# Kernel optimization log

Measured on AMD Instinct MI355X. Metric: run time of the kernel, lower is better.

Reference implementation:

```python
import jax, jax.numpy as jnp
import numpy as np

D = 256        # model_dim
E = 4          # num_experts
H = 8          # attention heads
L = 8          # layers
P = 4          # patch size
IMG = 128
B = 8
NUM_CLASSES = 10
T = (IMG // P) ** 2  # 1024 tokens


def _ln(x, g, b):
    mu = jnp.mean(x, -1, keepdims=True)
    var = jnp.mean((x - mu) ** 2, -1, keepdims=True)
    return (x - mu) * jax.lax.rsqrt(var + 1e-5) * g + b


def setup_inputs() -> dict:
    key = jax.random.key(0)
    ks = jax.random.split(key, 24)
    n = lambda k, s, sc=0.02: jax.random.normal(k, s, jnp.float32) * sc
    return {
        "x": jax.random.normal(ks[0], (B, 3, IMG, IMG), jnp.float32),
        "patch_w": n(ks[1], (D, 3, P, P), 0.1),
        "patch_b": n(ks[2], (D,), 0.01),
        "pos_emb": n(ks[3], (1, T, D), 0.02),
        "router_w": n(ks[4], (E, D), 0.05),
        "router_b": n(ks[5], (E,), 0.01),
        "ln1_g": jnp.ones((L, D), jnp.float32),
        "ln1_b": jnp.zeros((L, D), jnp.float32),
        "q_w": n(ks[6], (L, D, D), 0.05),
        "q_b": n(ks[7], (L, D), 0.01),
        "k_w": n(ks[8], (L, D, D), 0.05),
        "k_b": n(ks[9], (L, D), 0.01),
        "v_w": n(ks[10], (L, D, D), 0.05),
        "v_b": n(ks[11], (L, D), 0.01),
        "o_w": n(ks[12], (L, D, D), 0.05),
        "o_b": n(ks[13], (L, D), 0.01),
        "ln2_g": jnp.ones((L, D), jnp.float32),
        "ln2_b": jnp.zeros((L, D), jnp.float32),
        "l1_w": n(ks[14], (L, 4 * D, D), 0.05),
        "l1_b": n(ks[15], (L, 4 * D), 0.01),
        "l2_w": n(ks[16], (L, D, 4 * D), 0.05),
        "l2_b": n(ks[17], (L, D), 0.01),
        "head_w": n(ks[18], (NUM_CLASSES, D), 0.05),
        "head_b": n(ks[19], (NUM_CLASSES,), 0.01),
        "alpha": jnp.full((1,), 0.5, jnp.float32),
    }


def reference(x, patch_w, patch_b, pos_emb, router_w, router_b, ln1_g, ln1_b,
              q_w, q_b, k_w, k_b, v_w, v_b, o_w, o_b, ln2_g, ln2_b,
              l1_w, l1_b, l2_w, l2_b, head_w, head_b, alpha):
    b = x.shape[0]
    # patch embed: Conv2d(3, D, P, stride=P)
    h = jax.lax.conv_general_dilated(x, patch_w, (P, P), 'VALID',
                                     dimension_numbers=('NCHW', 'OIHW', 'NCHW'))
    h = h + patch_b[None, :, None, None]
    tok = h.reshape(b, D, -1).transpose(0, 2, 1) + pos_emb   # [B,T,D]
    t = tok.shape[1]
    n_per = t // E  # uniform capacity: floor(T * 1/E)
    raw_prob = jax.nn.softmax(tok @ router_w.T + router_b, axis=-1)  # [B,T,E]
    # greedy routing: expert e takes top n_per of remaining tokens, rows zeroed after
    prob = raw_prob
    bidx = jnp.arange(b)[:, None]
    blocks, pblocks = [], []
    for e in range(E):
        _, idx = jax.lax.top_k(prob[:, :, e], n_per)            # [B,n_per]
        blocks.append(jnp.take_along_axis(tok, idx[:, :, None], axis=1))
        pblocks.append(jnp.take_along_axis(raw_prob, idx[:, :, None], axis=1))
        sel = jnp.zeros((b, t), prob.dtype).at[bidx, idx].set(1.0)
        prob = prob * (1.0 - sel)[:, :, None]
    xs = jnp.concatenate(blocks, axis=1)    # [B,T,D] expert-sorted
    rp = jnp.concatenate(pblocks, axis=1)   # [B,T,E]

    widths = [D // 2 ** e for e in range(E)]  # [256,128,64,32]
    scale = D ** -0.5                         # note: model_dim, not head_dim
    dh = D // H
    for l in range(L):
        # ---- nested-expert MHSA ----
        xn = _ln(xs, ln1_g[l], ln1_b[l])
        qs, ks_, vs = [], [], []
        for e in range(E):
            m = widths[e]
            blk = xn[:, e * n_per:(e + 1) * n_per, :m]
            qs.append(blk @ q_w[l][:, :m].T + q_b[l])
            ks_.append(blk @ k_w[l][:, :m].T + k_b[l])
            vs.append(blk @ v_w[l][:, :m].T + v_b[l])
        q = jnp.concatenate(qs, 1).reshape(b, t, H, dh).transpose(0, 2, 1, 3)
        k = jnp.concatenate(ks_, 1).reshape(b, t, H, dh).transpose(0, 2, 1, 3)
        v = jnp.concatenate(vs, 1).reshape(b, t, H, dh).transpose(0, 2, 1, 3)
        attn = jax.nn.softmax(jnp.einsum('bhqd,bhkd->bhqk', q, k) * scale, axis=-1)
        ao = jnp.einsum('bhqk,bhkd->bhqd', attn, v).transpose(0, 2, 1, 3).reshape(b, t, D)
        outs = []
        for e in range(E):
            m = widths[e]
            sl = slice(e * n_per, (e + 1) * n_per)
            o = ao[:, sl, :m] @ o_w[l][:m, :m].T + o_b[l][:m]
            o = jnp.pad(o, ((0, 0), (0, 0), (0, D - m)))
            outs.append(o + xs[:, sl, :])
        xs = jnp.concatenate(outs, 1)
        # ---- nested-expert MLP ----
        xn = _ln(xs, ln2_g[l], ln2_b[l])
        outs = []
        for e in range(E):
            m = widths[e]
            sl = slice(e * n_per, (e + 1) * n_per)
            blk = xn[:, sl, :m]
            inner = jax.nn.gelu(blk @ l1_w[l][:, :m].T + l1_b[l], approximate=False)
            outer = inner @ l2_w[l][:m, :].T + l2_b[l][:m]
            outer = jnp.pad(outer, ((0, 0), (0, 0), (0, D - m)))
            sf = (alpha[0] * rp[:, sl, e] + 1.0)[:, :, None]
            outs.append(xs[:, sl, :] + sf * outer)
        xs = jnp.concatenate(outs, 1)
    # classification head: mean pool + linear
    return jnp.mean(xs, axis=1) @ head_w.T + head_b
```

## Files before the change

kernel.cpp:

```cpp
#include <hip/hip_runtime.h>
#include <math.h>

#define D 256
#define E 4
#define H 8
#define LYR 8
#define IMG 128
#define BB 8
#define NC 10
#define T 1024
#define NPER 256
#define DH 32
#define D4 1024

using bf16x8 = __attribute__((ext_vector_type(8))) __bf16;
using bf16x4 = __attribute__((ext_vector_type(4))) __bf16;
using f32x4  = __attribute__((ext_vector_type(4))) float;

#define MFMA16(a, b, c) __builtin_amdgcn_mfma_f32_16x16x32_bf16((a), (b), (c), 0, 0, 0)
#define EXP2F(x) __builtin_exp2f(x)

__device__ __forceinline__ void gload16(const void* g, void* l) {
    __builtin_amdgcn_global_load_lds(
        (const __attribute__((address_space(1))) void*)g,
        (__attribute__((address_space(3))) void*)l, 16, 0, 0);
}

__global__ void cast6(const float* __restrict__ s0, const float* __restrict__ s1,
                      const float* __restrict__ s2, const float* __restrict__ s3,
                      const float* __restrict__ s4, const float* __restrict__ s5,
                      __bf16* __restrict__ d0, __bf16* __restrict__ d1,
                      __bf16* __restrict__ d2, __bf16* __restrict__ d3,
                      __bf16* __restrict__ d4, __bf16* __restrict__ d5) {
    const long A4 = (long)LYR * D * D / 4;
    const long W4 = (long)LYR * D4 * D / 4;
    long i = (long)blockIdx.x * 256 + threadIdx.x;
    const float* s; __bf16* d; long off;
    if (i < 4 * A4) {
        int w = (int)(i / A4); off = i - (long)w * A4;
        s = w == 0 ? s0 : w == 1 ? s1 : w == 2 ? s2 : s3;
        d = w == 0 ? d0 : w == 1 ? d1 : w == 2 ? d2 : d3;
    } else {
        long j = i - 4 * A4;
        int w = (int)(j / W4); off = j - (long)w * W4;
        s = w ? s5 : s4; d = w ? d5 : d4;
    }
    float4 v = ((const float4*)s)[off];
    bf16x4 o;
    o[0] = (__bf16)v.x; o[1] = (__bf16)v.y; o[2] = (__bf16)v.z; o[3] = (__bf16)v.w;
    ((bf16x4*)d)[off] = o;
}

__global__ void patch_router(const float* __restrict__ x, const float* __restrict__ pw,
                             const float* __restrict__ pb, const float* __restrict__ pos,
                             const float* __restrict__ rw, const float* __restrict__ rb,
                             float* __restrict__ tok, float* __restrict__ rawp) {
    int t = blockIdx.x, b = blockIdx.y, d = threadIdx.x;
    __shared__ float sx[48];
    __shared__ float srow[D];
    __shared__ float slog[4];
    int ph = t >> 5, pwc = t & 31;
    if (d < 48) {
        int c = d >> 4, ij = d & 15, i = ij >> 2, j = ij & 3;
        sx[d] = x[(((long)b * 3 + c) * IMG + (ph * 4 + i)) * IMG + (pwc * 4 + j)];
    }
    __syncthreads();
    float acc = pb[d];
    #pragma unroll
    for (int kk = 0; kk < 48; ++kk) acc += sx[kk] * pw[d * 48 + kk];
    float val = acc + pos[(long)t * D + d];
    tok[((long)b * T + t) * D + d] = val;
    srow[d] = val;
    __syncthreads();
    int wv = d >> 6, lane = d & 63;
    float a = 0.f;
    for (int c = lane; c < D; c += 64) a += srow[c] * rw[wv * D + c];
    for (int off = 32; off; off >>= 1) a += __shfl_down(a, off);
    if (lane == 0) slog[wv] = a + rb[wv];
    __syncthreads();
    if (d == 0) {
        float l0 = slog[0], l1 = slog[1], l2 = slog[2], l3 = slog[3];
        float mx = fmaxf(fmaxf(l0, l1), fmaxf(l2, l3));
        float e0 = __expf(l0 - mx), e1 = __expf(l1 - mx), e2 = __expf(l2 - mx), e3 = __expf(l3 - mx);
        float inv = 1.0f / (e0 + e1 + e2 + e3);
        long row = (long)b * T + t;
        rawp[row * 4 + 0] = e0 * inv;
        rawp[row * 4 + 1] = e1 * inv;
        rawp[row * 4 + 2] = e2 * inv;
        rawp[row * 4 + 3] = e3 * inv;
    }
}

__global__ __launch_bounds__(1024) void route_topk(const float* __restrict__ rawp,
                                                   int* __restrict__ perm,
                                                   float* __restrict__ rpsel) {
    int b = blockIdx.x, tid = threadIdx.x;
    int lane = tid & 63, wv = tid >> 6;
    __shared__ unsigned hist[256];
    __shared__ unsigned long long ball[16];
    __shared__ int sb_bin, sb_rem;
    bool assigned = false;
    for (int e = 0; e < E; ++e) {
        float v = rawp[((long)b * T + tid) * E + e];
        unsigned key = assigned ? 0u : __float_as_uint(v);
        unsigned prefix = 0;
        int rem = NPER;
        #pragma unroll
        for (int pass = 3; pass >= 0; --pass) {
            int shift = pass * 8;
            if (tid < 256) hist[tid] = 0;
            __syncthreads();
            bool active = (pass == 3) || ((key >> (shift + 8)) == prefix);
            if (active) atomicAdd(&hist[(key >> shift) & 255], 1u);
            __syncthreads();
            if (tid < 64) {
                unsigned c[4], psum = 0;
                #pragma unroll
                for (int u = 0; u < 4; ++u) { c[u] = hist[tid * 4 + u]; psum += c[u]; }
                unsigned suf = psum;
                #pragma unroll
                for (int off = 1; off < 64; off <<= 1) {
                    unsigned o = __shfl_down(suf, off);
                    if (tid + off < 64) suf += o;
                }
                unsigned El = suf - psum;
                if (El < (unsigned)rem && (unsigned)rem <= suf) {
                    unsigned cab = El;
                    #pragma unroll
                    for (int u = 3; u >= 0; --u) {
                        if ((unsigned)rem > cab && (unsigned)rem <= cab + c[u]) {
                            sb_bin = tid * 4 + u;
                            sb_rem = (int)((unsigned)rem - cab);
                        }
                        cab += c[u];
                    }
                }
            }
            __syncthreads();
            prefix = (prefix << 8) | (unsigned)sb_bin;
            rem = sb_rem;
        }
        unsigned t = prefix;
        bool is_tie = (!assigned) && (key == t);
        unsigned long long mbt = __ballot(is_tie);
        if (lane == 0) ball[wv] = mbt;
        __syncthreads();
        int tierank = 0;
        for (int w2 = 0; w2 < wv; ++w2) tierank += __popcll(ball[w2]);
        tierank += __popcll(mbt & ((1ULL << lane) - 1));
        bool sel = (!assigned) && ((key > t) || (is_tie && tierank < rem));
        __syncthreads();
        unsigned long long mbs = __ballot(sel);
        if (lane == 0) ball[wv] = mbs;
        __syncthreads();
        int rank = 0;
        for (int w2 = 0; w2 < wv; ++w2) rank += __popcll(ball[w2]);
        rank += __popcll(mbs & ((1ULL << lane) - 1));
        if (sel) {
            perm[(long)b * T + e * NPER + rank] = tid;
            rpsel[(long)b * T + e * NPER + rank] = v;
            assigned = true;
        }
        __syncthreads();
    }
}

__global__ void gather_tokens(const float* __restrict__ tok, const int* __restrict__ perm,
                              float* __restrict__ xs) {
    int slot = blockIdx.x, b = blockIdx.y, d = threadIdx.x;
    int src = perm[(long)b * T + slot];
    xs[((long)b * T + slot) * D + d] = tok[((long)b * T + src) * D + d];
}

__device__ __forceinline__ void ln_rows32(const float* __restrict__ src,
                                          const float* __restrict__ g,
                                          const float* __restrict__ bta,
                                          __bf16 (*slds)[264], int tid) {
    int sub = tid & 15, rowh = tid >> 4;
    int col0 = sub * 16;
    float gv[16], bv[16];
    #pragma unroll
    for (int u = 0; u < 4; ++u) {
        float4 gg = *(const float4*)&g[col0 + 4 * u];
        float4 bb = *(const float4*)&bta[col0 + 4 * u];
        gv[4*u] = gg.x; gv[4*u+1] = gg.y; gv[4*u+2] = gg.z; gv[4*u+3] = gg.w;
        bv[4*u] = bb.x; bv[4*u+1] = bb.y; bv[4*u+2] = bb.z; bv[4*u+3] = bb.w;
    }
    #pragma unroll
    for (int half = 0; half < 2; ++half) {
        int r = rowh + half * 16;
        const float* rp = src + (long)r * D + col0;
        float v[16];
        #pragma unroll
        for (int u = 0; u < 4; ++u) {
            float4 vv = *(const float4*)&rp[4 * u];
            v[4*u] = vv.x; v[4*u+1] = vv.y; v[4*u+2] = vv.z; v[4*u+3] = vv.w;
        }
        float s = 0.f;
        #pragma unroll
        for (int u = 0; u < 16; ++u) s += v[u];
        #pragma unroll
        for (int mk = 1; mk < 16; mk <<= 1) s += __shfl_xor(s, mk);
        float mu = s * (1.0f / D);
        float s2 = 0.f;
        #pragma unroll
        for (int u = 0; u < 16; ++u) { v[u] -= mu; s2 += v[u] * v[u]; }
        #pragma unroll
        for (int mk = 1; mk < 16; mk <<= 1) s2 += __shfl_xor(s2, mk);
        float rstd = rsqrtf(s2 * (1.0f / D) + 1e-5f);
        bf16x8 o0, o1;
        #pragma unroll
        for (int u = 0; u < 8; ++u) o0[u] = (__bf16)(v[u] * rstd * gv[u] + bv[u]);
        #pragma unroll
        for (int u = 0; u < 8; ++u) o1[u] = (__bf16)(v[8+u] * rstd * gv[8+u] + bv[8+u]);
        *(bf16x8*)&slds[r][col0]     = o0;
        *(bf16x8*)&slds[r][col0 + 8] = o1;
    }
}

template<int RG, int NG, int K>
__device__ __forceinline__ void gemm_tile(
    const __bf16* __restrict__ A, int lda,
    const __bf16* __restrict__ W, int ldb,
    int lane, f32x4 (&acc)[RG][NG])
{
    int lr = lane & 15, lk = (lane >> 4) * 8;
    const __bf16* a0 = A + (long)lr * lda + lk;
    const __bf16* b0 = W + (long)lr * ldb + lk;
    constexpr int CH = (K <= 256) ? K : 128;
    for (int kb = 0; kb < K; kb += CH) {
        #pragma unroll
        for (int ku = 0; ku < CH; ku += 32) {
            int k = kb + ku;
            bf16x8 av[RG], bv[NG];
            #pragma unroll
            for (int i = 0; i < RG; ++i) av[i] = *(const bf16x8*)(a0 + i * 16 * lda + k);
            #pragma unroll
            for (int n = 0; n < NG; ++n) bv[n] = *(const bf16x8*)(b0 + (long)n * 16 * ldb + k);
            #pragma unroll
            for (int i = 0; i < RG; ++i)
                #pragma unroll
                for (int n = 0; n < NG; ++n)
                    acc[i][n] = MFMA16(av[i], bv[n], acc[i][n]);
        }
    }
}

#define GEMM_K_DISPATCH(RG, NG, Aexpr, lda, Wexpr, ldb, accv)                         \
    switch (m) {                                                                      \
      case 256: gemm_tile<RG, NG, 256>(Aexpr, lda, Wexpr, ldb, lane, accv); break;    \
      case 128: gemm_tile<RG, NG, 128>(Aexpr, lda, Wexpr, ldb, lane, accv); break;    \
      case 64:  gemm_tile<RG, NG, 64>(Aexpr, lda, Wexpr, ldb, lane, accv); break;     \
      default:  gemm_tile<RG, NG, 32>(Aexpr, lda, Wexpr, ldb, lane, accv); break;     \
    }

__device__ __forceinline__ void tile_map32(int tau, int& e, int& rt, int& ct) {
    if (tau < 128)      { e = 0; rt = tau >> 3; ct = tau & 7; }
    else if (tau < 192) { e = 1; int t2 = tau - 128; rt = t2 >> 2; ct = t2 & 3; }
    else if (tau < 224) { e = 2; int t2 = tau - 192; rt = t2 >> 1; ct = t2 & 1; }
    else                { e = 3; rt = tau - 224; ct = 0; }
}

__global__ __launch_bounds__(512) void qkv_ln_gemm(
    const float* __restrict__ xs,
    const __bf16* __restrict__ qwb, const __bf16* __restrict__ kwb, const __bf16* __restrict__ vwb,
    const float* __restrict__ qb, const float* __restrict__ kb, const float* __restrict__ vb,
    const float* __restrict__ g, const float* __restrict__ bta,
    __bf16* __restrict__ Qb, __bf16* __restrict__ Kb, __bf16* __restrict__ Vt)
{
    int tid = threadIdx.x, lane = tid & 63, wid = tid >> 6;
    int tile = blockIdx.x, b = blockIdx.y;
    int row0 = tile * 32;
    int m = D >> (row0 >> 8);
    __shared__ __bf16 slds[32][264];
    if (tid < 256) ln_rows32(xs + ((long)b * T + row0) * D, g, bta, slds, tid);
    __syncthreads();
    int lr = lane & 15, rg = (lane >> 4) * 4;
    const f32x4 vz = {0.f, 0.f, 0.f, 0.f};
    for (int t = wid; t < 12; t += 8) {
        int which = t >> 2;
        int ncol0 = (t & 3) * 64;
        const __bf16* W = which == 0 ? qwb : which == 1 ? kwb : vwb;
        const float* bias = which == 0 ? qb : which == 1 ? kb : vb;
        f32x4 acc[2][4];
        #pragma unroll
        for (int i = 0; i < 2; ++i) { acc[i][0]=vz; acc[i][1]=vz; acc[i][2]=vz; acc[i][3]=vz; }
        GEMM_K_DISPATCH(2, 4, &slds[0][0], 264, W + (long)ncol0 * D, D, acc)
        #pragma unroll
        for (int i = 0; i < 2; ++i) {
            int row = row0 + i * 16 + rg;
            #pragma unroll
            for (int j = 0; j < 4; ++j) {
                int n = ncol0 + j * 16 + lr;
                float bvs = bias[n];
                if (which == 2) {
                    bf16x4 pk;
                    #pragma unroll
                    for (int r = 0; r < 4; ++r) pk[r] = (__bf16)(acc[i][j][r] + bvs);
                    *(bf16x4*)&Vt[((long)b * D + n) * T + row] = pk;
                } else if (which == 0) {
                    #pragma unroll
                    for (int r = 0; r < 4; ++r)
                        Qb[((long)b * T + row + r) * D + n] =
                            (__bf16)((acc[i][j][r] + bvs) * 0.09016844005556f);
                } else {
                    #pragma unroll
                    for (int r = 0; r < 4; ++r)
                        Kb[((long)b * T + row + r) * D + n] = (__bf16)(acc[i][j][r] + bvs);
                }
            }
        }
    }
}

__global__ __launch_bounds__(128) void attn_mfma(
    const __bf16* __restrict__ Qb, const __bf16* __restrict__ Kb,
    const __bf16* __restrict__ Vt, __bf16* __restrict__ aob)
{
    int bid = blockIdx.x;
    int bh = (bid & 7) * 8 + ((bid >> 3) & 7);
    int qt = bid >> 6;
    int b = bh >> 3, h = bh & 7;
    int tid = threadIdx.x;
    int lane = tid & 63, wave = tid >> 6;
    int lr = lane & 15, g = lane >> 4;
    int q0 = qt * 64 + wave * 32;
    __shared__ __bf16 plds[2][32][72];
    __shared__ __bf16 sK[2][4 * 64 * 8];
    __shared__ __bf16 sV[2][4 * 64 * 8];
    const f32x4 vz = {0.f, 0.f, 0.f, 0.f};
    bf16x8 qf[2];
    qf[0] = *(const bf16x8*)&Qb[((long)b * T + q0 + lr) * D + h * DH + g * 8];
    qf[1] = *(const bf16x8*)&Qb[((long)b * T + q0 + 16 + lr) * D + h * DH + g * 8];
    bf16x8 ones;
    #pragma unroll
    for (int u = 0; u < 8; ++u) ones[u] = (__bf16)1.0f;
    f32x4 acc[2][2] = {{vz, vz}, {vz, vz}};
    f32x4 accs[2] = {vz, vz};
    int j0 = 2 * wave, j1 = 2 * wave + 1;
    const __bf16* kseg0 = Kb + ((long)b * T + 16 * j0 + lr) * D + h * DH + g * 8;
    const __bf16* kseg1 = Kb + ((long)b * T + 16 * j1 + lr) * D + h * DH + g * 8;
    const __bf16* vseg0 = Vt + ((long)b * D + h * DH + (j0 >> 1) * 16 + lr) * T
                             + 32 * (j0 & 1) + 8 * g;
    const __bf16* vseg1 = Vt + ((long)b * D + h * DH + (j1 >> 1) * 16 + lr) * T
                             + 32 * (j1 & 1) + 8 * g;

#define STAGE(BSEL, KC)                                        \
    {                                                          \
        gload16(kseg0 + (long)(KC) * D, &sK[BSEL][j0 * 512]);  \
        gload16(kseg1 + (long)(KC) * D, &sK[BSEL][j1 * 512]);  \
        gload16(vseg0 + (KC),           &sV[BSEL][j0 * 512]);  \
        gload16(vseg1 + (KC),           &sV[BSEL][j1 * 512]);  \
    }

#define COMPUTE(BSEL)                                                                     \
    {                                                                                     \
        bf16x8 kf[4], vf[2][2];                                                           \
        _Pragma("unroll")                                                                 \
        for (int j = 0; j < 4; ++j)                                                       \
            kf[j] = *(const bf16x8*)&sK[BSEL][(j * 64 + lane) * 8];                       \
        _Pragma("unroll")                                                                 \
        for (int w2 = 0; w2 < 2; ++w2)                                                    \
            _Pragma("unroll")                                                             \
            for (int df = 0; df < 2; ++df)                                                \
                vf[w2][df] = *(const bf16x8*)&sV[BSEL][((df * 2 + w2) * 64 + lane) * 8];  \
        _Pragma("unroll")                                                                 \
        for (int qi = 0; qi < 2; ++qi) {                                                  \
            _Pragma("unroll")                                                             \
            for (int j = 0; j < 4; ++j) {                                                 \
                f32x4 s = MFMA16(kf[j], qf[qi], vz);                                      \
                float p0 = EXP2F(s[0]), p1 = EXP2F(s[1]);                                 \
                float p2 = EXP2F(s[2]), p3 = EXP2F(s[3]);                                 \
                bf16x4 pk;                                                                \
                pk[0] = (__bf16)p0; pk[1] = (__bf16)p1;                                   \
                pk[2] = (__bf16)p2; pk[3] = (__bf16)p3;                                   \
                *(bf16x4*)&plds[wave][qi * 16 + lr][16 * j + 4 * g] = pk;                 \
            }                                                                             \
        }                                                                                 \
        _Pragma("unroll")                                                                 \
        for (int qi = 0; qi < 2; ++qi) {                                                  \
            _Pragma("unroll")                                                             \
            for (int w2 = 0; w2 < 2; ++w2) {                                              \
                bf16x8 pa = *(const bf16x8*)&plds[wave][qi * 16 + lr][32 * w2 + 8 * g];   \
                acc[qi][0] = MFMA16(pa, vf[w2][0], acc[qi][0]);                           \
                acc[qi][1] = MFMA16(pa, vf[w2][1], acc[qi][1]);                           \
                accs[qi]   = MFMA16(pa, ones,     accs[qi]);                              \
            }                                                                             \
        }                                                                                 \
    }

    STAGE(0, 0)
    __syncthreads();
    int bsel = 0;
    for (int kc = 0; kc < T; kc += 64) {
        if (kc + 64 < T) STAGE(bsel ^ 1, kc + 64)
        COMPUTE(bsel)
        __syncthreads();
        bsel ^= 1;
    }
#undef STAGE
#undef COMPUTE

    #pragma unroll
    for (int qi = 0; qi < 2; ++qi) {
        #pragma unroll
        for (int r = 0; r < 4; ++r) {
            float inv = 1.0f / accs[qi][r];
            long obase = ((long)b * T + q0 + qi * 16 + 4 * g + r) * D + h * DH;
            aob[obase + lr]      = (__bf16)(acc[qi][0][r] * inv);
            aob[obase + 16 + lr] = (__bf16)(acc[qi][1][r] * inv);
        }
    }
}

__global__ __launch_bounds__(256) void oproj_gemm(
    const __bf16* __restrict__ aob, const __bf16* __restrict__ owb,
    const float* __restrict__ ob, float* __restrict__ xs)
{
    int tid = threadIdx.x, lane = tid & 63, wid = tid >> 6;
    int gw = blockIdx.x * 4 + wid;
    int b = gw / 240, tau = gw % 240;
    int e, rt, ct;
    tile_map32(tau, e, rt, ct);
    int m = D >> e;
    int row0 = e * NPER + rt * 16;
    int ncol0 = ct * 32;
    const f32x4 vz = {0.f, 0.f, 0.f, 0.f};
    f32x4 acc[1][2] = {{vz, vz}};
    GEMM_K_DISPATCH(1, 2, aob + ((long)b * T + row0) * D, D, owb + (long)ncol0 * D, D, acc)
    int lr = lane & 15, rg = (lane >> 4) * 4;
    int row = row0 + rg;
    #pragma unroll
    for (int j = 0; j < 2; ++j) {
        int n = ncol0 + j * 16 + lr;
        float bv = ob[n];
        #pragma unroll
        for (int r = 0; r < 4; ++r)
            xs[((long)b * T + row + r) * D + n] += acc[0][j][r] + bv;
    }
}

__global__ __launch_bounds__(256) void mlp1_ln_gemm(
    const float* __restrict__ xs, const __bf16* __restrict__ w1b,
    const float* __restrict__ b1, const float* __restrict__ g, const float* __restrict__ bta,
    __bf16* __restrict__ innerb)
{
    int tid = threadIdx.x, lane = tid & 63, wid = tid >> 6;
    int tile = blockIdx.x, fq = blockIdx.y, b = blockIdx.z;
    int row0 = tile * 32;
    int m = D >> (row0 >> 8);
    __shared__ __bf16 slds[32][264];
    ln_rows32(xs + ((long)b * T + row0) * D, g, bta, slds, tid);
    __syncthreads();
    int ncol0 = fq * 256 + wid * 64;
    const f32x4 vz = {0.f, 0.f, 0.f, 0.f};
    f32x4 acc[2][4];
    #pragma unroll
    for (int i = 0; i < 2; ++i) { acc[i][0]=vz; acc[i][1]=vz; acc[i][2]=vz; acc[i][3]=vz; }
    GEMM_K_DISPATCH(2, 4, &slds[0][0], 264, w1b + (long)ncol0 * D, D, acc)
    int lr = lane & 15, rg = (lane >> 4) * 4;
    #pragma unroll
    for (int i = 0; i < 2; ++i) {
        int row = row0 + i * 16 + rg;
        #pragma unroll
        for (int j = 0; j < 4; ++j) {
            int f = ncol0 + j * 16 + lr;
            float bv = b1[f];
            #pragma unroll
            for (int r = 0; r < 4; ++r) {
                float xv = acc[i][j][r] + bv;
                float gl = 0.5f * xv * (1.0f + erff(xv * 0.70710678118654752f));
                innerb[((long)b * T + row + r) * D4 + f] = (__bf16)gl;
            }
        }
    }
}

__global__ __launch_bounds__(256) void mlp2_gemm(
    const __bf16* __restrict__ innerb, const __bf16* __restrict__ w2b,
    const float* __restrict__ b2, const float* __restrict__ rpsel,
    const float* __restrict__ alpha, float* __restrict__ xs)
{
    int tid = threadIdx.x, lane = tid & 63, wid = tid >> 6;
    int gw = blockIdx.x * 4 + wid;
    int b = gw / 240, tau = gw % 240;
    int e, rt, ct;
    tile_map32(tau, e, rt, ct);
    int row0 = e * NPER + rt * 16;
    int ncol0 = ct * 32;
    const f32x4 vz = {0.f, 0.f, 0.f, 0.f};
    f32x4 acc[1][2] = {{vz, vz}};
    gemm_tile<1, 2, 1024>(innerb + ((long)b * T + row0) * D4, D4,
                          w2b + (long)ncol0 * D4, D4, lane, acc);
    int lr = lane & 15, rg = (lane >> 4) * 4;
    int row = row0 + rg;
    float a0 = alpha[0];
    float sf[4];
    #pragma unroll
    for (int r = 0; r < 4; ++r) sf[r] = a0 * rpsel[(long)b * T + row + r] + 1.0f;
    #pragma unroll
    for (int j = 0; j < 2; ++j) {
        int n = ncol0 + j * 16 + lr;
        float bv = b2[n];
        #pragma unroll
        for (int r = 0; r < 4; ++r)
            xs[((long)b * T + row + r) * D + n] += sf[r] * (acc[0][j][r] + bv);
    }
}

__global__ void head_partial(const float* __restrict__ xs, float* __restrict__ part) {
    int c = blockIdx.x, b = blockIdx.y, d = threadIdx.x;
    const float* p = xs + ((long)b * T + c * 128) * D + d;
    float s = 0.f;
    #pragma unroll 8
    for (int i = 0; i < 128; ++i) s += p[(long)i * D];
    part[((long)b * 8 + c) * D + d] = s;
}

__global__ void head_final(const float* __restrict__ part, const float* __restrict__ hw,
                           const float* __restrict__ hb, float* __restrict__ out) {
    int b = blockIdx.x, d = threadIdx.x;
    __shared__ float smean[D];
    float s = 0.f;
    #pragma unroll
    for (int c = 0; c < 8; ++c) s += part[((long)b * 8 + c) * D + d];
    smean[d] = s * (1.0f / T);
    __syncthreads();
    if (d < NC) {
        float acc = hb[d];
        for (int c = 0; c < D; ++c) acc += smean[c] * hw[d * D + c];
        out[b * NC + d] = acc;
    }
}

extern "C" void kernel_launch(void* const* d_in, const int* in_sizes, int n_in,
                              void* d_out, int out_size, void* d_ws, size_t ws_size,
                              hipStream_t stream) {
    const float* x      = (const float*)d_in[0];
    const float* patchw = (const float*)d_in[1];
    const float* patchb = (const float*)d_in[2];
    const float* pos    = (const float*)d_in[3];
    const float* rw     = (const float*)d_in[4];
    const float* rb     = (const float*)d_in[5];
    const float* ln1g   = (const float*)d_in[6];
    const float* ln1b   = (const float*)d_in[7];
    const float* qw     = (const float*)d_in[8];
    const float* qbi    = (const float*)d_in[9];
    const float* kw     = (const float*)d_in[10];
    const float* kbi    = (const float*)d_in[11];
    const float* vw     = (const float*)d_in[12];
    const float* vbi    = (const float*)d_in[13];
    const float* ow     = (const float*)d_in[14];
    const float* obi    = (const float*)d_in[15];
    const float* ln2g   = (const float*)d_in[16];
    const float* ln2b   = (const float*)d_in[17];
    const float* l1w    = (const float*)d_in[18];
    const float* l1b    = (const float*)d_in[19];
    const float* l2w    = (const float*)d_in[20];
    const float* l2b    = (const float*)d_in[21];
    const float* hw     = (const float*)d_in[22];
    const float* hb     = (const float*)d_in[23];
    const float* alpha  = (const float*)d_in[24];

    char* p = (char*)d_ws;
    auto alloc = [&](size_t bytes) { void* r = (void*)p; p += (bytes + 255) & ~(size_t)255; return r; };
    const long NTD = (long)BB * T * D;

    float*  tok    = (float*)alloc(NTD * 4);
    float*  xs     = (float*)alloc(NTD * 4);
    float*  rawp   = (float*)alloc((long)BB * T * E * 4);
    float*  rpsel  = (float*)alloc((long)BB * T * 4);
    int*    perm   = (int*)alloc((long)BB * T * 4);
    float*  part   = (float*)alloc((long)BB * 8 * D * 4);
    __bf16* Qb     = (__bf16*)alloc(NTD * 2);
    __bf16* Kb     = (__bf16*)alloc(NTD * 2);
    __bf16* Vt     = (__bf16*)alloc(NTD * 2);
    __bf16* aob    = (__bf16*)alloc(NTD * 2);
    __bf16* innerb = (__bf16*)alloc((long)BB * T * D4 * 2);
    __bf16* qwb    = (__bf16*)alloc((long)LYR * D * D * 2);
    __bf16* kwb    = (__bf16*)alloc((long)LYR * D * D * 2);
    __bf16* vwb    = (__bf16*)alloc((long)LYR * D * D * 2);
    __bf16* owb    = (__bf16*)alloc((long)LYR * D * D * 2);
    __bf16* w1b    = (__bf16*)alloc((long)LYR * D4 * D * 2);
    __bf16* w2b    = (__bf16*)alloc((long)LYR * D * D4 * 2);

    cast6<<<6144, 256, 0, stream>>>(qw, kw, vw, ow, l1w, l2w, qwb, kwb, vwb, owb, w1b, w2b);

    patch_router<<<dim3(T, BB), 256, 0, stream>>>(x, patchw, patchb, pos, rw, rb, tok, rawp);
    route_topk<<<BB, 1024, 0, stream>>>(rawp, perm, rpsel);
    gather_tokens<<<dim3(T, BB), 256, 0, stream>>>(tok, perm, xs);

    for (int l = 0; l < LYR; ++l) {
        qkv_ln_gemm<<<dim3(32, BB), 512, 0, stream>>>(
            xs, qwb + (long)l * D * D, kwb + (long)l * D * D, vwb + (long)l * D * D,
            qbi + l * D, kbi + l * D, vbi + l * D,
            ln1g + l * D, ln1b + l * D, Qb, Kb, Vt);
        attn_mfma<<<dim3(1024), 128, 0, stream>>>(Qb, Kb, Vt, aob);
        oproj_gemm<<<dim3(480), 256, 0, stream>>>(
            aob, owb + (long)l * D * D, obi + l * D, xs);
        mlp1_ln_gemm<<<dim3(32, 4, BB), 256, 0, stream>>>(
            xs, w1b + (long)l * D4 * D, l1b + (long)l * D4,
            ln2g + l * D, ln2b + l * D, innerb);
        mlp2_gemm<<<dim3(480), 256, 0, stream>>>(
            innerb, w2b + (long)l * D * D4, l2b + l * D, rpsel, alpha, xs);
    }

    head_partial<<<dim3(8, BB), 256, 0, stream>>>(xs, part);
    head_final<<<BB, D, 0, stream>>>(part, hw, hb, (float*)d_out);
}
```

Before: 954.4 us.

## Use single-wave attention blocks and replace barriers with waitcnt sync

```diff
diff --git a/kernel.cpp b/kernel.cpp
--- a/kernel.cpp
+++ b/kernel.cpp
@@ -313,7 +313,7 @@
     }
 }
 
-__global__ __launch_bounds__(128) void attn_mfma(
+__global__ __launch_bounds__(64) void attn_mfma(
     const __bf16* __restrict__ Qb, const __bf16* __restrict__ Kb,
     const __bf16* __restrict__ Vt, __bf16* __restrict__ aob)
 {
@@ -321,13 +321,12 @@
     int bh = (bid & 7) * 8 + ((bid >> 3) & 7);
     int qt = bid >> 6;
     int b = bh >> 3, h = bh & 7;
-    int tid = threadIdx.x;
-    int lane = tid & 63, wave = tid >> 6;
+    int lane = threadIdx.x;
     int lr = lane & 15, g = lane >> 4;
-    int q0 = qt * 64 + wave * 32;
-    __shared__ __bf16 plds[2][32][72];
-    __shared__ __bf16 sK[2][4 * 64 * 8];
-    __shared__ __bf16 sV[2][4 * 64 * 8];
+    int q0 = qt * 32;
+    __shared__ __bf16 plds[32][72];
+    __shared__ __bf16 sK[2][2048];
+    __shared__ __bf16 sV[2][2048];
     const f32x4 vz = {0.f, 0.f, 0.f, 0.f};
     bf16x8 qf[2];
     qf[0] = *(const bf16x8*)&Qb[((long)b * T + q0 + lr) * D + h * DH + g * 8];
@@ -337,20 +336,25 @@
     for (int u = 0; u < 8; ++u) ones[u] = (__bf16)1.0f;
     f32x4 acc[2][2] = {{vz, vz}, {vz, vz}};
     f32x4 accs[2] = {vz, vz};
-    int j0 = 2 * wave, j1 = 2 * wave + 1;
-    const __bf16* kseg0 = Kb + ((long)b * T + 16 * j0 + lr) * D + h * DH + g * 8;
-    const __bf16* kseg1 = Kb + ((long)b * T + 16 * j1 + lr) * D + h * DH + g * 8;
-    const __bf16* vseg0 = Vt + ((long)b * D + h * DH + (j0 >> 1) * 16 + lr) * T
-                             + 32 * (j0 & 1) + 8 * g;
-    const __bf16* vseg1 = Vt + ((long)b * D + h * DH + (j1 >> 1) * 16 + lr) * T
-                             + 32 * (j1 & 1) + 8 * g;
-
-#define STAGE(BSEL, KC)                                        \
-    {                                                          \
-        gload16(kseg0 + (long)(KC) * D, &sK[BSEL][j0 * 512]);  \
-        gload16(kseg1 + (long)(KC) * D, &sK[BSEL][j1 * 512]);  \
-        gload16(vseg0 + (KC),           &sV[BSEL][j0 * 512]);  \
-        gload16(vseg1 + (KC),           &sV[BSEL][j1 * 512]);  \
+    const __bf16* ks0 = Kb + ((long)b * T +  0 + lr) * D + h * DH + g * 8;
+    const __bf16* ks1 = Kb + ((long)b * T + 16 + lr) * D + h * DH + g * 8;
+    const __bf16* ks2 = Kb + ((long)b * T + 32 + lr) * D + h * DH + g * 8;
+    const __bf16* ks3 = Kb + ((long)b * T + 48 + lr) * D + h * DH + g * 8;
+    const __bf16* vs0 = Vt + ((long)b * D + h * DH +  0 + lr) * T +  0 + 8 * g;
+    const __bf16* vs1 = Vt + ((long)b * D + h * DH +  0 + lr) * T + 32 + 8 * g;
+    const __bf16* vs2 = Vt + ((long)b * D + h * DH + 16 + lr) * T +  0 + 8 * g;
+    const __bf16* vs3 = Vt + ((long)b * D + h * DH + 16 + lr) * T + 32 + 8 * g;
+
+#define STAGE(BSEL, KC)                                   \
+    {                                                     \
+        gload16(ks0 + (long)(KC) * D, &sK[BSEL][0]);      \
+        gload16(ks1 + (long)(KC) * D, &sK[BSEL][512]);    \
+        gload16(ks2 + (long)(KC) * D, &sK[BSEL][1024]);   \
+        gload16(ks3 + (long)(KC) * D, &sK[BSEL][1536]);   \
+        gload16(vs0 + (KC), &sV[BSEL][0]);                \
+        gload16(vs1 + (KC), &sV[BSEL][512]);              \
+        gload16(vs2 + (KC), &sV[BSEL][1024]);             \
+        gload16(vs3 + (KC), &sV[BSEL][1536]);             \
     }
 
 #define COMPUTE(BSEL)                                                                     \
@@ -374,14 +378,14 @@
                 bf16x4 pk;                                                                \
                 pk[0] = (__bf16)p0; pk[1] = (__bf16)p1;                                   \
                 pk[2] = (__bf16)p2; pk[3] = (__bf16)p3;                                   \
-                *(bf16x4*)&plds[wave][qi * 16 + lr][16 * j + 4 * g] = pk;                 \
+                *(bf16x4*)&plds[qi * 16 + lr][16 * j + 4 * g] = pk;                       \
             }                                                                             \
         }                                                                                 \
         _Pragma("unroll")                                                                 \
         for (int qi = 0; qi < 2; ++qi) {                                                  \
             _Pragma("unroll")                                                             \
             for (int w2 = 0; w2 < 2; ++w2) {                                              \
-                bf16x8 pa = *(const bf16x8*)&plds[wave][qi * 16 + lr][32 * w2 + 8 * g];   \
+                bf16x8 pa = *(const bf16x8*)&plds[qi * 16 + lr][32 * w2 + 8 * g];         \
                 acc[qi][0] = MFMA16(pa, vf[w2][0], acc[qi][0]);                           \
                 acc[qi][1] = MFMA16(pa, vf[w2][1], acc[qi][1]);                           \
                 accs[qi]   = MFMA16(pa, ones,     accs[qi]);                              \
@@ -390,12 +394,18 @@
     }
 
     STAGE(0, 0)
-    __syncthreads();
     int bsel = 0;
     for (int kc = 0; kc < T; kc += 64) {
-        if (kc + 64 < T) STAGE(bsel ^ 1, kc + 64)
+        if (kc + 64 < T) {
+            STAGE(bsel ^ 1, kc + 64)
+            asm volatile("s_waitcnt vmcnt(8)" ::: "memory");
+        } else {
+            asm volatile("s_waitcnt vmcnt(0)" ::: "memory");
+        }
+        __builtin_amdgcn_sched_barrier(0);
         COMPUTE(bsel)
-        __syncthreads();
+        asm volatile("s_waitcnt lgkmcnt(0)" ::: "memory");
+        __builtin_amdgcn_sched_barrier(0);
         bsel ^= 1;
     }
 #undef STAGE
@@ -595,7 +605,7 @@
             xs, qwb + (long)l * D * D, kwb + (long)l * D * D, vwb + (long)l * D * D,
             qbi + l * D, kbi + l * D, vbi + l * D,
             ln1g + l * D, ln1b + l * D, Qb, Kb, Vt);
-        attn_mfma<<<dim3(1024), 128, 0, stream>>>(Qb, Kb, Vt, aob);
+        attn_mfma<<<dim3(2048), 64, 0, stream>>>(Qb, Kb, Vt, aob);
         oproj_gemm<<<dim3(480), 256, 0, stream>>>(
             aob, owb + (long)l * D * D, obi + l * D, xs);
         mlp1_ln_gemm<<<dim3(32, 4, BB), 256, 0, stream>>>(
```

Result: slower. 1.094 ms (+14.6%).
